# Optimization experiments

Hardware: AMD Instinct MI355X
Metric: run time of the kernel (lower is better)

The kernel has to match this reference:

```python
import jax, jax.numpy as jnp
import numpy as np

N, E, D = 50000, 800000, 256

def setup_inputs() -> dict:
    key = jax.random.key(0)
    ks = jax.random.split(key, 12)
    s = 1.0 / np.sqrt(D)
    return {
        "x": jax.random.normal(ks[0], (N, D), dtype=jnp.float32),
        "src": jax.random.randint(ks[1], (E,), 0, N, dtype=jnp.int64),
        "dst": jax.random.randint(ks[2], (E,), 0, N, dtype=jnp.int64),
        "W_w": jax.random.normal(ks[3], (D, D), dtype=jnp.float32) * s,
        "W_b": jnp.zeros((D,), dtype=jnp.float32),
        "U_w": jax.random.normal(ks[4], (D, D), dtype=jnp.float32) * s,
        "U_b": jnp.zeros((D,), dtype=jnp.float32),
        "V_w": jax.random.normal(ks[5], (D, D), dtype=jnp.float32) * s,
        "V_b": jnp.zeros((D,), dtype=jnp.float32),
        "attn_l": jax.random.normal(ks[6], (D,), dtype=jnp.float32) * s,
        "attn_r": jax.random.normal(ks[7], (D,), dtype=jnp.float32) * s,
        "gamma": jnp.ones((D,), dtype=jnp.float32),
        "beta": jnp.zeros((D,), dtype=jnp.float32),
    }

def reference(x, src, dst, W_w, W_b, U_w, U_b, V_w, V_b, attn_l, attn_r, gamma, beta):
    # node transforms (dropout p=0 -> identity)
    Wh = x @ W_w + W_b            # [N, D]
    Uh = x @ U_w + U_b            # [N, D]
    Vh = x @ V_w + V_b            # [N, D]
    out_src = Wh * attn_l         # [N, D]
    out_dst = Wh * attn_r         # [N, D]
    # per-edge gate: sigma = sigmoid(out_src[u] + out_dst[v])  [E, D]
    sigma = jax.nn.sigmoid(out_src[src] + out_dst[dst])
    # aggregate to destination nodes
    sum_sigma_h = jax.ops.segment_sum(Vh[src] * sigma, dst, num_segments=N)
    sum_sigma = jax.ops.segment_sum(sigma, dst, num_segments=N)
    h = Uh + sum_sigma_h / (sum_sigma + 1e-6)
    # layer norm (eps=1e-6, affine)
    mu = jnp.mean(h, axis=-1, keepdims=True)
    var = jnp.mean((h - mu) ** 2, axis=-1, keepdims=True)
    h = (h - mu) / jnp.sqrt(var + 1e-6) * gamma + beta
    h = jax.nn.relu(h)
    return x + h  # residual
```

## Files before the change

kernel.cpp:

```cpp
#include <hip/hip_runtime.h>
#include <hip/hip_bf16.h>

#define NN 50000
#define NE 800000
#define NB 196
#define NROWPAD 50048

#define XCVT_BLOCKS 6250
#define TW_BLOCKS   192
#define HIST_BLOCKS 3125
#define GEMM_NWG    2346

#if __has_builtin(__builtin_amdgcn_cvt_pk_fp8_f32) && __has_builtin(__builtin_amdgcn_cvt_pk_f32_fp8)
#define HAVE_FP8 1
#define ROWB 768
#else
#define HAVE_FP8 0
#define ROWB 1024
#endif

typedef __attribute__((ext_vector_type(8))) short short8;
typedef __attribute__((ext_vector_type(4))) float floatx4;
typedef __attribute__((ext_vector_type(2))) float floatx2;
typedef unsigned short u16;
typedef unsigned int u32;

__device__ __forceinline__ u16 f2bf(float f) {
    u32 u = __float_as_uint(f);
    u += 0x7FFFu + ((u >> 16) & 1u);
    return (u16)(u >> 16);
}
__device__ __forceinline__ float bf_lo(u32 u) { return __uint_as_float(u << 16); }
__device__ __forceinline__ float bf_hi(u32 u) { return __uint_as_float(u & 0xFFFF0000u); }
__device__ __forceinline__ u32 pack_bf(float lo, float hi) {
    return (u32)f2bf(lo) | ((u32)f2bf(hi) << 16);
}

#if __has_builtin(__builtin_amdgcn_exp2f)
#define EXP2F(x) __builtin_amdgcn_exp2f(x)
#else
#define EXP2F(x) exp2f(x)
#endif

__global__ __launch_bounds__(256) void prep_kernel(
    const float* __restrict__ x, u16* __restrict__ xbf,
    const float* __restrict__ W, const float* __restrict__ U, const float* __restrict__ V,
    u16* __restrict__ wT, const int* __restrict__ dst, int* __restrict__ deg, int do_xcvt) {
    __shared__ float s[32][33];
    int b = blockIdx.x;
    int xb = do_xcvt ? XCVT_BLOCKS : 0;
    if (b < xb) {
        size_t i = ((size_t)b * 256 + threadIdx.x) * 8;
        floatx4 f0 = *(const floatx4*)(x + i);
        floatx4 f1 = *(const floatx4*)(x + i + 4);
        uint4 pk;
        pk.x = pack_bf(f0[0], f0[1]);
        pk.y = pack_bf(f0[2], f0[3]);
        pk.z = pack_bf(f1[0], f1[1]);
        pk.w = pack_bf(f1[2], f1[3]);
        *(uint4*)(xbf + i) = pk;
    } else if (b < xb + TW_BLOCKS) {
        int bb = b - xb;
        int g = bb >> 6, rem = bb & 63;
        int r0 = (rem & 7) * 32, c0 = (rem >> 3) * 32;
        const float* M = (g == 0) ? W : ((g == 1) ? U : V);
        int tx = threadIdx.x & 31, ty = threadIdx.x >> 5;
#pragma unroll
        for (int k = 0; k < 4; ++k)
            s[ty + k * 8][tx] = M[(size_t)(r0 + ty + k * 8) * 256 + c0 + tx];
        __syncthreads();
#pragma unroll
        for (int k = 0; k < 4; ++k)
            wT[(size_t)(g * 256 + c0 + ty + k * 8) * 256 + r0 + tx] = f2bf(s[tx][ty + k * 8]);
    } else {
        int e = (b - xb - TW_BLOCKS) * 256 + threadIdx.x;
        if (e < NE) atomicAdd(&deg[dst[e]], 1);
    }
}

__global__ __launch_bounds__(256) void scanA_kernel(const int* __restrict__ deg, int* __restrict__ bsum) {
    int t = threadIdx.x;
    int i = blockIdx.x * 256 + t;
    int v = (i < NN) ? deg[i] : 0;
#pragma unroll
    for (int m = 32; m; m >>= 1) v += __shfl_xor(v, m, 64);
    __shared__ int ws[4];
    if ((t & 63) == 0) ws[t >> 6] = v;
    __syncthreads();
    if (t == 0) bsum[blockIdx.x] = ws[0] + ws[1] + ws[2] + ws[3];
}

__global__ __launch_bounds__(256) void scanB_kernel(const int* __restrict__ bsum, int* __restrict__ bpre,
                                                    int* __restrict__ rows_end) {
    int t = threadIdx.x, lane = t & 63, wv = t >> 6;
    int v = (t < NB) ? bsum[t] : 0;
    int inc = v;
#pragma unroll
    for (int off = 1; off < 64; off <<= 1) {
        int u = __shfl_up(inc, off, 64);
        if (lane >= off) inc += u;
    }
    __shared__ int wsum[4];
    if (lane == 63) wsum[wv] = inc;
    __syncthreads();
    int woff = 0;
    for (int k = 0; k < wv; ++k) woff += wsum[k];
    if (t < NB) bpre[t] = woff + inc - v;
    if (t == 255) rows_end[0] = woff + inc;
}

__global__ __launch_bounds__(256) void scanC_kernel(const int* __restrict__ deg, const int* __restrict__ bpre,
                                                    int* __restrict__ rows, int* __restrict__ cursor) {
    int t = threadIdx.x, lane = t & 63, wv = t >> 6;
    int i = blockIdx.x * 256 + t;
    int v = (i < NN) ? deg[i] : 0;
    int inc = v;
#pragma unroll
    for (int off = 1; off < 64; off <<= 1) {
        int u = __shfl_up(inc, off, 64);
        if (lane >= off) inc += u;
    }
    __shared__ int wsum[4];
    if (lane == 63) wsum[wv] = inc;
    __syncthreads();
    int woff = bpre[blockIdx.x];
    for (int k = 0; k < wv; ++k) woff += wsum[k];
    int excl = woff + inc - v;
    if (i < NN) { rows[i] = excl; cursor[i] = excl; }
}

__global__ void scatter_kernel(const int* __restrict__ src, const int* __restrict__ dst,
                               int* __restrict__ cursor, int* __restrict__ esrc) {
    int e = blockIdx.x * 256 + threadIdx.x;
    if (e < NE) {
        int d = dst[e];
        int pos = atomicAdd(&cursor[d], 1);
        esrc[pos] = src[e];
    }
}

template<bool USE_BF>
__global__ __launch_bounds__(256, 2) void gemm3_kernel(
    const u16* __restrict__ xbf, const float* __restrict__ xf, const u16* __restrict__ wT,
    const float* __restrict__ Wb, const float* __restrict__ Ub, const float* __restrict__ Vb,
    char* __restrict__ WVh, float* __restrict__ Uh) {
    int orig = blockIdx.x;
    int xcd = orig & 7, j = orig >> 3;
    int wgid = (xcd < 2 ? xcd * 294 : 2 * 294 + (xcd - 2) * 293) + j;
    int rb = (wgid / 6) * 128;
    int cgy = wgid % 6;
    int cbg = cgy * 128;

    int t = threadIdx.x, lane = t & 63, w = t >> 6;

    int arow = rb + w * 32 + (lane & 15);
    short8 afr[2][8];
    if (USE_BF) {
#pragma unroll
        for (int rg = 0; rg < 2; ++rg)
#pragma unroll
            for (int ks = 0; ks < 8; ++ks)
                afr[rg][ks] = *(const short8*)(xbf + (size_t)(arow + rg * 16) * 256 + ks * 32 + (lane >> 4) * 8);
    } else {
#pragma unroll
        for (int rg = 0; rg < 2; ++rg)
#pragma unroll
            for (int ks = 0; ks < 8; ++ks) {
                int row = arow + rg * 16;
                const float* p = xf + ((size_t)(row < NN ? row : 0)) * 256 + ks * 32 + (lane >> 4) * 8;
                floatx4 f0 = *(const floatx4*)(p);
                floatx4 f1 = *(const floatx4*)(p + 4);
                uint4 pk;
                pk.x = pack_bf(f0[0], f0[1]);
                pk.y = pack_bf(f0[2], f0[3]);
                pk.z = pack_bf(f1[0], f1[1]);
                pk.w = pack_bf(f1[2], f1[3]);
                afr[rg][ks] = *(short8*)&pk;
            }
    }

    const u16* wTb = wT + (size_t)(cbg + (lane & 15)) * 256 + (lane >> 4) * 8;
    floatx4 acc[2][8] = {};
#pragma unroll
    for (int ks = 0; ks < 8; ++ks) {
#pragma unroll
        for (int cf = 0; cf < 8; ++cf) {
            short8 bfrag = *(const short8*)(wTb + (size_t)cf * 16 * 256 + ks * 32);
            acc[0][cf] = __builtin_amdgcn_mfma_f32_16x16x32_bf16(bfrag, afr[0][ks], acc[0][cf], 0, 0, 0);
            acc[1][cf] = __builtin_amdgcn_mfma_f32_16x16x32_bf16(bfrag, afr[1][ks], acc[1][cf], 0, 0, 0);
        }
    }

    int g = cgy >> 1;
    int cloc = (cgy & 1) * 128;
    const float* bias = (g == 0) ? Wb : ((g == 1) ? Ub : Vb);

#pragma unroll
    for (int rg = 0; rg < 2; ++rg) {
        int noderow = rb + w * 32 + rg * 16 + (lane & 15);
        if (noderow >= NN) continue;
#pragma unroll
        for (int cf = 0; cf < 8; ++cf) {
            int colc = cloc + cf * 16 + (lane >> 4) * 4;
            floatx4 bv = *(const floatx4*)(bias + colc);
            float v0 = acc[rg][cf][0] + bv[0];
            float v1 = acc[rg][cf][1] + bv[1];
            float v2 = acc[rg][cf][2] + bv[2];
            float v3 = acc[rg][cf][3] + bv[3];
            if (g == 1) {
                floatx4 o = { v0, v1, v2, v3 };
                *(floatx4*)(Uh + (size_t)noderow * 256 + colc) = o;
            } else if (g == 0) {
#if HAVE_FP8
                u32 p = 0;
                p = __builtin_amdgcn_cvt_pk_fp8_f32(v0, v1, p, false);
                p = __builtin_amdgcn_cvt_pk_fp8_f32(v2, v3, p, true);
                *(u32*)(WVh + (size_t)noderow * ROWB + colc) = p;
#else
                uint2 o = { pack_bf(v0, v1), pack_bf(v2, v3) };
                *(uint2*)(WVh + (size_t)noderow * ROWB + colc * 2) = o;
#endif
            } else {
#if HAVE_FP8
                uint2 o = { pack_bf(v0, v1), pack_bf(v2, v3) };
                *(uint2*)(WVh + (size_t)noderow * ROWB + 256 + colc * 2) = o;
#else
                uint2 o = { pack_bf(v0, v1), pack_bf(v2, v3) };
                *(uint2*)(WVh + (size_t)noderow * ROWB + 512 + colc * 2) = o;
#endif
            }
        }
    }
}

__global__ __launch_bounds__(256) void node_kernel(
    const char* __restrict__ WVh, const float* __restrict__ x,
    const int* __restrict__ rows, const int* __restrict__ esrc,
    const float* __restrict__ attn_l, const float* __restrict__ attn_r,
    const float* __restrict__ gamma, const float* __restrict__ beta,
    float* inout) {
    int wv = threadIdx.x >> 6, lane = threadIdx.x & 63;
    int v = blockIdx.x * 4 + wv;
    if (v >= NN) return;
    int c0 = lane * 4;

    const float NL2E = -1.44269504f;
    floatx4 alv = *(const floatx4*)(attn_l + c0);
    floatx4 arv = *(const floatx4*)(attn_r + c0);

    float mywf[4];
#if HAVE_FP8
    {
        u32 myw = *(const u32*)(WVh + (size_t)v * ROWB + lane * 4);
        floatx2 a = __builtin_amdgcn_cvt_pk_f32_fp8(myw, false);
        floatx2 b = __builtin_amdgcn_cvt_pk_f32_fp8(myw, true);
        mywf[0] = a[0]; mywf[1] = a[1]; mywf[2] = b[0]; mywf[3] = b[1];
    }
#else
    {
        uint2 myw = *(const uint2*)(WVh + (size_t)v * ROWB + lane * 8);
        mywf[0] = bf_lo(myw.x); mywf[1] = bf_hi(myw.x);
        mywf[2] = bf_lo(myw.y); mywf[3] = bf_hi(myw.y);
    }
#endif
    float al2[4] = { alv[0] * NL2E, alv[1] * NL2E, alv[2] * NL2E, alv[3] * NL2E };
    float td2[4] = { mywf[0] * arv[0] * NL2E, mywf[1] * arv[1] * NL2E,
                     mywf[2] * arv[2] * NL2E, mywf[3] * arv[3] * NL2E };

    float acc_h[4] = {0.f, 0.f, 0.f, 0.f};
    float acc_s[4] = {0.f, 0.f, 0.f, 0.f};

#if HAVE_FP8
    auto edge = [&](u32 w8, uint2 vu) {
        floatx2 a = __builtin_amdgcn_cvt_pk_f32_fp8(w8, false);
        floatx2 b = __builtin_amdgcn_cvt_pk_f32_fp8(w8, true);
        float wf[4] = { a[0], a[1], b[0], b[1] };
        float vf[4] = { bf_lo(vu.x), bf_hi(vu.x), bf_lo(vu.y), bf_hi(vu.y) };
#pragma unroll
        for (int j = 0; j < 4; ++j) {
            float m = fmaf(wf[j], al2[j], td2[j]);
            float s = __builtin_amdgcn_rcpf(1.0f + EXP2F(m));
            acc_s[j] += s;
            acc_h[j] = fmaf(s, vf[j], acc_h[j]);
        }
    };
    int e = rows[v], e1 = rows[v + 1];
    for (; e + 8 <= e1; e += 8) {
        int us[8];
#pragma unroll
        for (int q = 0; q < 8; ++q) us[q] = esrc[e + q];
        u32 w8[8]; uint2 vu[8];
#pragma unroll
        for (int q = 0; q < 8; ++q) {
            const char* p = WVh + (size_t)us[q] * ROWB;
            w8[q] = *(const u32*)(p + lane * 4);
            vu[q] = *(const uint2*)(p + 256 + lane * 8);
        }
#pragma unroll
        for (int q = 0; q < 8; ++q) edge(w8[q], vu[q]);
    }
    for (; e < e1; ++e) {
        const char* p = WVh + (size_t)esrc[e] * ROWB;
        edge(*(const u32*)(p + lane * 4), *(const uint2*)(p + 256 + lane * 8));
    }
#else
    auto edge = [&](uint2 wu, uint2 vu) {
        float wf[4] = { bf_lo(wu.x), bf_hi(wu.x), bf_lo(wu.y), bf_hi(wu.y) };
        float vf[4] = { bf_lo(vu.x), bf_hi(vu.x), bf_lo(vu.y), bf_hi(vu.y) };
#pragma unroll
        for (int j = 0; j < 4; ++j) {
            float m = fmaf(wf[j], al2[j], td2[j]);
            float s = __builtin_amdgcn_rcpf(1.0f + EXP2F(m));
            acc_s[j] += s;
            acc_h[j] = fmaf(s, vf[j], acc_h[j]);
        }
    };
    int e = rows[v], e1 = rows[v + 1];
    for (; e + 8 <= e1; e += 8) {
        int us[8];
#pragma unroll
        for (int q = 0; q < 8; ++q) us[q] = esrc[e + q];
        uint2 wu[8], vu[8];
#pragma unroll
        for (int q = 0; q < 8; ++q) {
            const char* p = WVh + (size_t)us[q] * ROWB;
            wu[q] = *(const uint2*)(p + lane * 8);
            vu[q] = *(const uint2*)(p + 512 + lane * 8);
        }
#pragma unroll
        for (int q = 0; q < 8; ++q) edge(wu[q], vu[q]);
    }
    for (; e < e1; ++e) {
        const char* p = WVh + (size_t)esrc[e] * ROWB;
        edge(*(const uint2*)(p + lane * 8), *(const uint2*)(p + 512 + lane * 8));
    }
#endif

    floatx4 uh = *(const floatx4*)(inout + (size_t)v * 256 + c0);
    float h[4];
#pragma unroll
    for (int j = 0; j < 4; ++j)
        h[j] = uh[j] + acc_h[j] * __builtin_amdgcn_rcpf(acc_s[j] + 1e-6f);

    float s01 = h[0] + h[1] + h[2] + h[3];
#pragma unroll
    for (int m = 32; m; m >>= 1) s01 += __shfl_xor(s01, m, 64);
    float mu = s01 * (1.0f / 256.0f);
    float d[4] = { h[0] - mu, h[1] - mu, h[2] - mu, h[3] - mu };
    float sq = d[0] * d[0] + d[1] * d[1] + d[2] * d[2] + d[3] * d[3];
#pragma unroll
    for (int m = 32; m; m >>= 1) sq += __shfl_xor(sq, m, 64);
    float inv = rsqrtf(sq * (1.0f / 256.0f) + 1e-6f);

    floatx4 gm = *(const floatx4*)(gamma + c0);
    floatx4 bt = *(const floatx4*)(beta + c0);
    floatx4 xr = *(const floatx4*)(x + (size_t)v * 256 + c0);
    floatx4 res;
#pragma unroll
    for (int j = 0; j < 4; ++j) {
        float y = d[j] * inv * gm[j] + bt[j];
        y = fmaxf(y, 0.0f);
        res[j] = xr[j] + y;
    }
    *(floatx4*)(inout + (size_t)v * 256 + c0) = res;
}

extern "C" void kernel_launch(void* const* d_in, const int* in_sizes, int n_in,
                              void* d_out, int out_size, void* d_ws, size_t ws_size,
                              hipStream_t stream) {
    const float* x       = (const float*)d_in[0];
    const int*   src     = (const int*)d_in[1];
    const int*   dst     = (const int*)d_in[2];
    const float* W_w     = (const float*)d_in[3];
    const float* W_b     = (const float*)d_in[4];
    const float* U_w     = (const float*)d_in[5];
    const float* U_b     = (const float*)d_in[6];
    const float* V_w     = (const float*)d_in[7];
    const float* V_b     = (const float*)d_in[8];
    const float* attn_l  = (const float*)d_in[9];
    const float* attn_r  = (const float*)d_in[10];
    const float* gamma   = (const float*)d_in[11];
    const float* beta    = (const float*)d_in[12];

    char* ws = (char*)d_ws;
    size_t off = 0;
    auto alloc = [&](size_t bytes) -> char* {
        char* p = ws + off;
        off += (bytes + 255) & ~(size_t)255;
        return p;
    };
    char* WVh    = alloc((size_t)NN * ROWB);
    u16* wT      = (u16*)alloc((size_t)768 * 256 * 2);
    int* deg     = (int*)alloc((size_t)NN * 4);
    int* rows    = (int*)alloc((size_t)(NN + 1) * 4);
    int* cursor  = (int*)alloc((size_t)NN * 4);
    int* esrc    = (int*)alloc((size_t)NE * 4);
    int* bsum    = (int*)alloc((size_t)NB * 4);
    int* bpre    = (int*)alloc((size_t)NB * 4);
    u16* xbf     = (u16*)alloc((size_t)NROWPAD * 256 * 2);
    bool use_bf  = (ws_size >= off);

    float* Uh_f32 = (float*)d_out;

    hipMemsetAsync(deg, 0, (size_t)NN * 4, stream);

    int xb = use_bf ? XCVT_BLOCKS : 0;
    prep_kernel<<<xb + TW_BLOCKS + HIST_BLOCKS, 256, 0, stream>>>(
        x, xbf, W_w, U_w, V_w, wT, dst, deg, use_bf ? 1 : 0);

    scanA_kernel<<<NB, 256, 0, stream>>>(deg, bsum);
    scanB_kernel<<<1, 256, 0, stream>>>(bsum, bpre, rows + NN);
    scanC_kernel<<<NB, 256, 0, stream>>>(deg, bpre, rows, cursor);
    scatter_kernel<<<(NE + 255) / 256, 256, 0, stream>>>(src, dst, cursor, esrc);

    if (use_bf) {
        gemm3_kernel<true><<<GEMM_NWG, 256, 0, stream>>>(xbf, x, wT, W_b, U_b, V_b, WVh, Uh_f32);
    } else {
        gemm3_kernel<false><<<GEMM_NWG, 256, 0, stream>>>(nullptr, x, wT, W_b, U_b, V_b, WVh, Uh_f32);
    }

    node_kernel<<<(NN + 3) / 4, 256, 0, stream>>>(
        WVh, x, rows, esrc, attn_l, attn_r, gamma, beta, (float*)d_out);
}
```

Before: 316.3 us.

## Fuse edge scatter into GEMM launch and convert x to bf16 inline

Drops the separate x-to-bf16 conversion pass and its workspace buffer. The GEMM now reads fp32 x directly and converts it in registers. The edge scatter kernel is merged into the GEMM launch as leading blocks, so scatter and GEMM work can run concurrently and one launch is saved. The GEMM row tile shrinks from 128 to 64 rows per block with higher occupancy (launch bounds 4), and the XCD-aware block remapping is removed. The trade-off is more redundant fp32 reads of x (each row block is read by 6 column groups) and loss of the XCD locality mapping.

```diff
diff --git a/kernel.cpp b/kernel.cpp
--- a/kernel.cpp
+++ b/kernel.cpp
@@ -4,12 +4,12 @@
 #define NN 50000
 #define NE 800000
 #define NB 196
-#define NROWPAD 50048
-
-#define XCVT_BLOCKS 6250
+
 #define TW_BLOCKS   192
 #define HIST_BLOCKS 3125
-#define GEMM_NWG    2346
+#define SCAT_BLOCKS 3125
+#define GEMM_RB     782
+#define GEMM_BLOCKS (GEMM_RB * 6)
 
 #if __has_builtin(__builtin_amdgcn_cvt_pk_fp8_f32) && __has_builtin(__builtin_amdgcn_cvt_pk_f32_fp8)
 #define HAVE_FP8 1
@@ -43,25 +43,12 @@
 #endif
 
 __global__ __launch_bounds__(256) void prep_kernel(
-    const float* __restrict__ x, u16* __restrict__ xbf,
     const float* __restrict__ W, const float* __restrict__ U, const float* __restrict__ V,
-    u16* __restrict__ wT, const int* __restrict__ dst, int* __restrict__ deg, int do_xcvt) {
+    u16* __restrict__ wT, const int* __restrict__ dst, int* __restrict__ deg) {
     __shared__ float s[32][33];
     int b = blockIdx.x;
-    int xb = do_xcvt ? XCVT_BLOCKS : 0;
-    if (b < xb) {
-        size_t i = ((size_t)b * 256 + threadIdx.x) * 8;
-        floatx4 f0 = *(const floatx4*)(x + i);
-        floatx4 f1 = *(const floatx4*)(x + i + 4);
-        uint4 pk;
-        pk.x = pack_bf(f0[0], f0[1]);
-        pk.y = pack_bf(f0[2], f0[3]);
-        pk.z = pack_bf(f1[0], f1[1]);
-        pk.w = pack_bf(f1[2], f1[3]);
-        *(uint4*)(xbf + i) = pk;
-    } else if (b < xb + TW_BLOCKS) {
-        int bb = b - xb;
-        int g = bb >> 6, rem = bb & 63;
+    if (b < TW_BLOCKS) {
+        int g = b >> 6, rem = b & 63;
         int r0 = (rem & 7) * 32, c0 = (rem >> 3) * 32;
         const float* M = (g == 0) ? W : ((g == 1) ? U : V);
         int tx = threadIdx.x & 31, ty = threadIdx.x >> 5;
@@ -73,7 +60,7 @@
         for (int k = 0; k < 4; ++k)
             wT[(size_t)(g * 256 + c0 + ty + k * 8) * 256 + r0 + tx] = f2bf(s[tx][ty + k * 8]);
     } else {
-        int e = (b - xb - TW_BLOCKS) * 256 + threadIdx.x;
+        int e = (b - TW_BLOCKS) * 256 + threadIdx.x;
         if (e < NE) atomicAdd(&deg[dst[e]], 1);
     }
 }
@@ -129,106 +116,90 @@
     if (i < NN) { rows[i] = excl; cursor[i] = excl; }
 }
 
-__global__ void scatter_kernel(const int* __restrict__ src, const int* __restrict__ dst,
-                               int* __restrict__ cursor, int* __restrict__ esrc) {
-    int e = blockIdx.x * 256 + threadIdx.x;
-    if (e < NE) {
-        int d = dst[e];
-        int pos = atomicAdd(&cursor[d], 1);
-        esrc[pos] = src[e];
-    }
-}
-
-template<bool USE_BF>
-__global__ __launch_bounds__(256, 2) void gemm3_kernel(
-    const u16* __restrict__ xbf, const float* __restrict__ xf, const u16* __restrict__ wT,
+__global__ __launch_bounds__(256, 4) void gemm6_kernel(
+    const float* __restrict__ xf, const u16* __restrict__ wT,
     const float* __restrict__ Wb, const float* __restrict__ Ub, const float* __restrict__ Vb,
-    char* __restrict__ WVh, float* __restrict__ Uh) {
-    int orig = blockIdx.x;
-    int xcd = orig & 7, j = orig >> 3;
-    int wgid = (xcd < 2 ? xcd * 294 : 2 * 294 + (xcd - 2) * 293) + j;
-    int rb = (wgid / 6) * 128;
-    int cgy = wgid % 6;
+    char* __restrict__ WVh, float* __restrict__ Uh,
+    const int* __restrict__ src, const int* __restrict__ dst,
+    int* __restrict__ cursor, int* __restrict__ esrc) {
+    int b = blockIdx.x;
+    if (b < SCAT_BLOCKS) {
+        int e = b * 256 + threadIdx.x;
+        if (e < NE) {
+            int d = dst[e];
+            int pos = atomicAdd(&cursor[d], 1);
+            esrc[pos] = src[e];
+        }
+        return;
+    }
+    int gb = b - SCAT_BLOCKS;
+    int rb = (gb % GEMM_RB) * 64;
+    int cgy = gb / GEMM_RB;
     int cbg = cgy * 128;
 
     int t = threadIdx.x, lane = t & 63, w = t >> 6;
 
-    int arow = rb + w * 32 + (lane & 15);
-    short8 afr[2][8];
-    if (USE_BF) {
-#pragma unroll
-        for (int rg = 0; rg < 2; ++rg)
-#pragma unroll
-            for (int ks = 0; ks < 8; ++ks)
-                afr[rg][ks] = *(const short8*)(xbf + (size_t)(arow + rg * 16) * 256 + ks * 32 + (lane >> 4) * 8);
-    } else {
-#pragma unroll
-        for (int rg = 0; rg < 2; ++rg)
-#pragma unroll
-            for (int ks = 0; ks < 8; ++ks) {
-                int row = arow + rg * 16;
-                const float* p = xf + ((size_t)(row < NN ? row : 0)) * 256 + ks * 32 + (lane >> 4) * 8;
-                floatx4 f0 = *(const floatx4*)(p);
-                floatx4 f1 = *(const floatx4*)(p + 4);
-                uint4 pk;
-                pk.x = pack_bf(f0[0], f0[1]);
-                pk.y = pack_bf(f0[2], f0[3]);
-                pk.z = pack_bf(f1[0], f1[1]);
-                pk.w = pack_bf(f1[2], f1[3]);
-                afr[rg][ks] = *(short8*)&pk;
-            }
+    int rw = rb + w * 16 + (lane & 15);
+    int rwc = min(rw, NN - 1);
+    const float* xp = xf + (size_t)rwc * 256 + (lane >> 4) * 8;
+    short8 afr[8];
+#pragma unroll
+    for (int ks = 0; ks < 8; ++ks) {
+        floatx4 f0 = *(const floatx4*)(xp + ks * 32);
+        floatx4 f1 = *(const floatx4*)(xp + ks * 32 + 4);
+        uint4 pk;
+        pk.x = pack_bf(f0[0], f0[1]);
+        pk.y = pack_bf(f0[2], f0[3]);
+        pk.z = pack_bf(f1[0], f1[1]);
+        pk.w = pack_bf(f1[2], f1[3]);
+        afr[ks] = *(short8*)&pk;
     }
 
     const u16* wTb = wT + (size_t)(cbg + (lane & 15)) * 256 + (lane >> 4) * 8;
-    floatx4 acc[2][8] = {};
+    floatx4 acc[8] = {};
 #pragma unroll
     for (int ks = 0; ks < 8; ++ks) {
 #pragma unroll
         for (int cf = 0; cf < 8; ++cf) {
             short8 bfrag = *(const short8*)(wTb + (size_t)cf * 16 * 256 + ks * 32);
-            acc[0][cf] = __builtin_amdgcn_mfma_f32_16x16x32_bf16(bfrag, afr[0][ks], acc[0][cf], 0, 0, 0);
-            acc[1][cf] = __builtin_amdgcn_mfma_f32_16x16x32_bf16(bfrag, afr[1][ks], acc[1][cf], 0, 0, 0);
-        }
-    }
-
+            acc[cf] = __builtin_amdgcn_mfma_f32_16x16x32_bf16(bfrag, afr[ks], acc[cf], 0, 0, 0);
+        }
+    }
+
+    if (rw >= NN) return;
     int g = cgy >> 1;
     int cloc = (cgy & 1) * 128;
     const float* bias = (g == 0) ? Wb : ((g == 1) ? Ub : Vb);
 
 #pragma unroll
-    for (int rg = 0; rg < 2; ++rg) {
-        int noderow = rb + w * 32 + rg * 16 + (lane & 15);
-        if (noderow >= NN) continue;
-#pragma unroll
-        for (int cf = 0; cf < 8; ++cf) {
-            int colc = cloc + cf * 16 + (lane >> 4) * 4;
-            floatx4 bv = *(const floatx4*)(bias + colc);
-            float v0 = acc[rg][cf][0] + bv[0];
-            float v1 = acc[rg][cf][1] + bv[1];
-            float v2 = acc[rg][cf][2] + bv[2];
-            float v3 = acc[rg][cf][3] + bv[3];
-            if (g == 1) {
-                floatx4 o = { v0, v1, v2, v3 };
-                *(floatx4*)(Uh + (size_t)noderow * 256 + colc) = o;
-            } else if (g == 0) {
+    for (int cf = 0; cf < 8; ++cf) {
+        int colc = cloc + cf * 16 + (lane >> 4) * 4;
+        floatx4 bv = *(const floatx4*)(bias + colc);
+        float v0 = acc[cf][0] + bv[0];
+        float v1 = acc[cf][1] + bv[1];
+        float v2 = acc[cf][2] + bv[2];
+        float v3 = acc[cf][3] + bv[3];
+        if (g == 1) {
+            floatx4 o = { v0, v1, v2, v3 };
+            *(floatx4*)(Uh + (size_t)rw * 256 + colc) = o;
+        } else if (g == 0) {
 #if HAVE_FP8
-                u32 p = 0;
-                p = __builtin_amdgcn_cvt_pk_fp8_f32(v0, v1, p, false);
-                p = __builtin_amdgcn_cvt_pk_fp8_f32(v2, v3, p, true);
-                *(u32*)(WVh + (size_t)noderow * ROWB + colc) = p;
-#else
-                uint2 o = { pack_bf(v0, v1), pack_bf(v2, v3) };
-                *(uint2*)(WVh + (size_t)noderow * ROWB + colc * 2) = o;
-#endif
-            } else {
+            u32 p = 0;
+            p = __builtin_amdgcn_cvt_pk_fp8_f32(v0, v1, p, false);
+            p = __builtin_amdgcn_cvt_pk_fp8_f32(v2, v3, p, true);
+            *(u32*)(WVh + (size_t)rw * ROWB + colc) = p;
+#else
+            uint2 o = { pack_bf(v0, v1), pack_bf(v2, v3) };
+            *(uint2*)(WVh + (size_t)rw * ROWB + colc * 2) = o;
+#endif
+        } else {
 #if HAVE_FP8
-                uint2 o = { pack_bf(v0, v1), pack_bf(v2, v3) };
-                *(uint2*)(WVh + (size_t)noderow * ROWB + 256 + colc * 2) = o;
-#else
-                uint2 o = { pack_bf(v0, v1), pack_bf(v2, v3) };
-                *(uint2*)(WVh + (size_t)noderow * ROWB + 512 + colc * 2) = o;
-#endif
-            }
+            uint2 o = { pack_bf(v0, v1), pack_bf(v2, v3) };
+            *(uint2*)(WVh + (size_t)rw * ROWB + 256 + colc * 2) = o;
+#else
+            uint2 o = { pack_bf(v0, v1), pack_bf(v2, v3) };
+            *(uint2*)(WVh + (size_t)rw * ROWB + 512 + colc * 2) = o;
+#endif
         }
     }
 }
@@ -397,27 +368,19 @@
     int* esrc    = (int*)alloc((size_t)NE * 4);
     int* bsum    = (int*)alloc((size_t)NB * 4);
     int* bpre    = (int*)alloc((size_t)NB * 4);
-    u16* xbf     = (u16*)alloc((size_t)NROWPAD * 256 * 2);
-    bool use_bf  = (ws_size >= off);
 
     float* Uh_f32 = (float*)d_out;
 
     hipMemsetAsync(deg, 0, (size_t)NN * 4, stream);
 
-    int xb = use_bf ? XCVT_BLOCKS : 0;
-    prep_kernel<<<xb + TW_BLOCKS + HIST_BLOCKS, 256, 0, stream>>>(
-        x, xbf, W_w, U_w, V_w, wT, dst, deg, use_bf ? 1 : 0);
+    prep_kernel<<<TW_BLOCKS + HIST_BLOCKS, 256, 0, stream>>>(W_w, U_w, V_w, wT, dst, deg);
 
     scanA_kernel<<<NB, 256, 0, stream>>>(deg, bsum);
     scanB_kernel<<<1, 256, 0, stream>>>(bsum, bpre, rows + NN);
     scanC_kernel<<<NB, 256, 0, stream>>>(deg, bpre, rows, cursor);
-    scatter_kernel<<<(NE + 255) / 256, 256, 0, stream>>>(src, dst, cursor, esrc);
-
-    if (use_bf) {
-        gemm3_kernel<true><<<GEMM_NWG, 256, 0, stream>>>(xbf, x, wT, W_b, U_b, V_b, WVh, Uh_f32);
-    } else {
-        gemm3_kernel<false><<<GEMM_NWG, 256, 0, stream>>>(nullptr, x, wT, W_b, U_b, V_b, WVh, Uh_f32);
-    }
+
+    gemm6_kernel<<<SCAT_BLOCKS + GEMM_BLOCKS, 256, 0, stream>>>(
+        x, wT, W_b, U_b, V_b, WVh, Uh_f32, src, dst, cursor, esrc);
 
     node_kernel<<<(NN + 3) / 4, 256, 0, stream>>>(
         WVh, x, rows, esrc, attn_l, attn_r, gamma, beta, (float*)d_out);
```

Result: slower. 379.7 us (+20.1%).

## Stage full weight matrix in LDS and enlarge GEMM tiles to 256x256

Applied to the files above, without the earlier changes.

The projection GEMM now uses 512-thread blocks that each cover 256 rows by 256 columns (one of W/U/V per grid y), with the whole 256x256 bf16 weight tile loaded into LDS via global_load_lds using an XOR swizzle. Before, B fragments were read straight from global memory, and the XCD-aware block remapping is dropped. The aim is to reuse weights from LDS instead of refetching them per fragment and to cut the number of blocks. The cost is 128KB of LDS per block, which limits occupancy, plus 64 accumulator registers per thread and far fewer blocks (588) to spread across CUs.

```diff
diff --git a/kernel.cpp b/kernel.cpp
--- a/kernel.cpp
+++ b/kernel.cpp
@@ -9,7 +9,6 @@
 #define XCVT_BLOCKS 6250
 #define TW_BLOCKS   192
 #define HIST_BLOCKS 3125
-#define GEMM_NWG    2346
 
 #if __has_builtin(__builtin_amdgcn_cvt_pk_fp8_f32) && __has_builtin(__builtin_amdgcn_cvt_pk_f32_fp8)
 #define HAVE_FP8 1
@@ -34,6 +33,10 @@
 __device__ __forceinline__ float bf_hi(u32 u) { return __uint_as_float(u & 0xFFFF0000u); }
 __device__ __forceinline__ u32 pack_bf(float lo, float hi) {
     return (u32)f2bf(lo) | ((u32)f2bf(hi) << 16);
+}
+__device__ __forceinline__ void gl_lds16(const void* g, void* l) {
+    __builtin_amdgcn_global_load_lds((const __attribute__((address_space(1))) void*)g,
+                                     (__attribute__((address_space(3))) void*)l, 16, 0, 0);
 }
 
 #if __has_builtin(__builtin_amdgcn_exp2f)
@@ -140,36 +143,46 @@
 }
 
 template<bool USE_BF>
-__global__ __launch_bounds__(256, 2) void gemm3_kernel(
+__global__ __launch_bounds__(512, 2) void gemm8_kernel(
     const u16* __restrict__ xbf, const float* __restrict__ xf, const u16* __restrict__ wT,
     const float* __restrict__ Wb, const float* __restrict__ Ub, const float* __restrict__ Vb,
     char* __restrict__ WVh, float* __restrict__ Uh) {
-    int orig = blockIdx.x;
-    int xcd = orig & 7, j = orig >> 3;
-    int wgid = (xcd < 2 ? xcd * 294 : 2 * 294 + (xcd - 2) * 293) + j;
-    int rb = (wgid / 6) * 128;
-    int cgy = wgid % 6;
-    int cbg = cgy * 128;
+    __shared__ __align__(16) u16 Bs[256 * 256];
+
+    int rb = blockIdx.x * 256;
+    int pass = blockIdx.y;
+    int cbg = pass * 256;
 
     int t = threadIdx.x, lane = t & 63, w = t >> 6;
 
-    int arow = rb + w * 32 + (lane & 15);
+#pragma unroll
+    for (int i = 0; i < 16; ++i) {
+        int slot = w * 16 + i;
+        int ci = slot * 2 + (lane >> 5);
+        int q = (lane & 31) ^ (ci & 7);
+        gl_lds16(wT + (size_t)(cbg + ci) * 256 + q * 8, Bs + slot * 512);
+    }
+
+    int arow0 = rb + w * 32 + (lane & 15);
     short8 afr[2][8];
     if (USE_BF) {
 #pragma unroll
-        for (int rg = 0; rg < 2; ++rg)
+        for (int rg = 0; rg < 2; ++rg) {
+            int row = min(arow0 + rg * 16, NN - 1);
+            const u16* p = xbf + (size_t)row * 256 + (lane >> 4) * 8;
 #pragma unroll
             for (int ks = 0; ks < 8; ++ks)
-                afr[rg][ks] = *(const short8*)(xbf + (size_t)(arow + rg * 16) * 256 + ks * 32 + (lane >> 4) * 8);
+                afr[rg][ks] = *(const short8*)(p + ks * 32);
+        }
     } else {
 #pragma unroll
-        for (int rg = 0; rg < 2; ++rg)
+        for (int rg = 0; rg < 2; ++rg) {
+            int row = min(arow0 + rg * 16, NN - 1);
+            const float* p = xf + (size_t)row * 256 + (lane >> 4) * 8;
 #pragma unroll
             for (int ks = 0; ks < 8; ++ks) {
-                int row = arow + rg * 16;
-                const float* p = xf + ((size_t)(row < NN ? row : 0)) * 256 + ks * 32 + (lane >> 4) * 8;
-                floatx4 f0 = *(const floatx4*)(p);
-                floatx4 f1 = *(const floatx4*)(p + 4);
+                floatx4 f0 = *(const floatx4*)(p + ks * 32);
+                floatx4 f1 = *(const floatx4*)(p + ks * 32 + 4);
                 uint4 pk;
                 pk.x = pack_bf(f0[0], f0[1]);
                 pk.y = pack_bf(f0[2], f0[3]);
@@ -177,40 +190,40 @@
                 pk.w = pack_bf(f1[2], f1[3]);
                 afr[rg][ks] = *(short8*)&pk;
             }
-    }
-
-    const u16* wTb = wT + (size_t)(cbg + (lane & 15)) * 256 + (lane >> 4) * 8;
-    floatx4 acc[2][8] = {};
+        }
+    }
+    __syncthreads();
+
+    floatx4 acc[2][16] = {};
 #pragma unroll
     for (int ks = 0; ks < 8; ++ks) {
 #pragma unroll
-        for (int cf = 0; cf < 8; ++cf) {
-            short8 bfrag = *(const short8*)(wTb + (size_t)cf * 16 * 256 + ks * 32);
+        for (int cf = 0; cf < 16; ++cf) {
+            int ci = cf * 16 + (lane & 15);
+            int q = (ks * 4 + (lane >> 4)) ^ (ci & 7);
+            short8 bfrag = *(const short8*)(Bs + ci * 256 + q * 8);
             acc[0][cf] = __builtin_amdgcn_mfma_f32_16x16x32_bf16(bfrag, afr[0][ks], acc[0][cf], 0, 0, 0);
             acc[1][cf] = __builtin_amdgcn_mfma_f32_16x16x32_bf16(bfrag, afr[1][ks], acc[1][cf], 0, 0, 0);
         }
     }
 
-    int g = cgy >> 1;
-    int cloc = (cgy & 1) * 128;
-    const float* bias = (g == 0) ? Wb : ((g == 1) ? Ub : Vb);
-
+    const float* bias = (pass == 0) ? Wb : ((pass == 1) ? Ub : Vb);
 #pragma unroll
     for (int rg = 0; rg < 2; ++rg) {
         int noderow = rb + w * 32 + rg * 16 + (lane & 15);
         if (noderow >= NN) continue;
 #pragma unroll
-        for (int cf = 0; cf < 8; ++cf) {
-            int colc = cloc + cf * 16 + (lane >> 4) * 4;
+        for (int cf = 0; cf < 16; ++cf) {
+            int colc = cf * 16 + (lane >> 4) * 4;
             floatx4 bv = *(const floatx4*)(bias + colc);
             float v0 = acc[rg][cf][0] + bv[0];
             float v1 = acc[rg][cf][1] + bv[1];
             float v2 = acc[rg][cf][2] + bv[2];
             float v3 = acc[rg][cf][3] + bv[3];
-            if (g == 1) {
+            if (pass == 1) {
                 floatx4 o = { v0, v1, v2, v3 };
                 *(floatx4*)(Uh + (size_t)noderow * 256 + colc) = o;
-            } else if (g == 0) {
+            } else if (pass == 0) {
 #if HAVE_FP8
                 u32 p = 0;
                 p = __builtin_amdgcn_cvt_pk_fp8_f32(v0, v1, p, false);
@@ -413,10 +426,11 @@
     scanC_kernel<<<NB, 256, 0, stream>>>(deg, bpre, rows, cursor);
     scatter_kernel<<<(NE + 255) / 256, 256, 0, stream>>>(src, dst, cursor, esrc);
 
+    dim3 gg(NB, 3);
     if (use_bf) {
-        gemm3_kernel<true><<<GEMM_NWG, 256, 0, stream>>>(xbf, x, wT, W_b, U_b, V_b, WVh, Uh_f32);
+        gemm8_kernel<true><<<gg, 512, 0, stream>>>(xbf, x, wT, W_b, U_b, V_b, WVh, Uh_f32);
     } else {
-        gemm3_kernel<false><<<GEMM_NWG, 256, 0, stream>>>(nullptr, x, wT, W_b, U_b, V_b, WVh, Uh_f32);
+        gemm8_kernel<false><<<gg, 512, 0, stream>>>(nullptr, x, wT, W_b, U_b, V_b, WVh, Uh_f32);
     }
 
     node_kernel<<<(NN + 3) / 4, 256, 0, stream>>>(
```

Result: faster. 273.2 us (median of 2 runs) (-13.6%).
